# Kernel optimization log

Measured on AMD Instinct MI355X. Metric: run time of the kernel, lower is better.

The kernel has to match this reference:

```python
import jax, jax.numpy as jnp
import numpy as np

B, C, H, W, HID = 4, 32, 256, 256, 64
EPS = 1e-5


def setup_inputs() -> dict:
    key = jax.random.key(0)
    ks = jax.random.split(key, 8)
    s = 0.05
    return {
        "x": jax.random.normal(ks[0], (B, C, H, W), jnp.float32),
        "Wqkv": jax.random.normal(ks[1], (3 * C, C), jnp.float32) * s,   # Conv2d 1x1, no bias
        "W1": jax.random.normal(ks[2], (HID, C), jnp.float32) * s,       # Linear(C -> HID)
        "b1": jnp.zeros((HID,), jnp.float32),
        "ln_w": jnp.ones((HID,), jnp.float32),
        "ln_b": jnp.zeros((HID,), jnp.float32),
        "W2": jax.random.normal(ks[3], (C, HID), jnp.float32) * s,       # Linear(HID -> C)
        "b2": jnp.zeros((C,), jnp.float32),
        "Wg": jax.random.normal(ks[4], (C, C), jnp.float32) * s,         # gate Conv2d 1x1
        "bg": jnp.zeros((C,), jnp.float32),
    }


def _unfold3x3(t):
    # t: (b, c, h, w) -> (b, c, 9, h, w), zero-padded 3x3 neighbors,
    # neighbor order matches F.unfold row-major kernel order.
    b, c, h, w = t.shape
    tp = jnp.pad(t, ((0, 0), (0, 0), (1, 1), (1, 1)))
    return jnp.stack(
        [tp[:, :, dy:dy + h, dx:dx + w] for dy in range(3) for dx in range(3)],
        axis=2,
    )


def reference(x, Wqkv, W1, b1, ln_w, ln_b, W2, b2, Wg, bg):
    b, c, h, w = x.shape
    qkv = jnp.einsum('oc,bchw->bohw', Wqkv, x)
    q, k, v = jnp.split(qkv, 3, axis=1)

    k_un = _unfold3x3(k)  # (b, c, 9, h, w)
    v_un = _unfold3x3(v)

    # (b, h, w, 9, c)
    q_minus_k = jnp.transpose(q[:, :, None] - k_un, (0, 3, 4, 2, 1))

    hid = jnp.einsum('bhwnc,dc->bhwnd', q_minus_k, W1) + b1
    mean = hid.mean(-1, keepdims=True)
    std = jnp.sqrt(((hid - mean) ** 2).mean(-1, keepdims=True))  # unbiased=False
    hid = ln_w * ((hid - mean) / (std + EPS)) + ln_b
    hid = jax.nn.relu(hid)
    scores = jnp.einsum('bhwnd,cd->bhwnc', hid, W2) + b2

    attn = jax.nn.softmax(scores, axis=-2)  # over neighbor dim (9)
    neighbors_v = jnp.transpose(v_un, (0, 3, 4, 2, 1))  # (b, h, w, 9, c)
    weighted_v = jnp.sum(neighbors_v * attn, axis=3)     # (b, h, w, c)
    weighted_v = jnp.transpose(weighted_v, (0, 3, 1, 2)) # (b, c, h, w)

    base = jnp.einsum('oc,bchw->bohw', Wg, x) + bg[None, :, None, None]
    return weighted_v + base + x
```

## Files before the change

kernel.cpp:

```cpp
#include <hip/hip_runtime.h>


#define HWm 65536
#define NPIX 262144
#define PW 258
#define PHW 66564
#define LOG2E 1.44269504088896340736f

typedef __attribute__((ext_vector_type(8))) _Float16 half8;
typedef __attribute__((ext_vector_type(2))) _Float16 half2v;
typedef __attribute__((ext_vector_type(4))) float f32x4;

__device__ __forceinline__ unsigned pkh(float a, float b) {
    auto h = __builtin_amdgcn_cvt_pkrtz(a, b);
    return __builtin_bit_cast(unsigned, h);
}
__device__ __forceinline__ half2v h2(unsigned u) { return __builtin_bit_cast(half2v, u); }

__global__ __launch_bounds__(256) void prep_kernel(
    const float* __restrict__ Wqkv, const float* __restrict__ W1,
    const float* __restrict__ W2, const float* __restrict__ b1v,
    const float* __restrict__ Wg, const float* __restrict__ bgv,
    const float* __restrict__ lnw, const float* __restrict__ lnb,
    const float* __restrict__ b2, float* __restrict__ Wk1,
    float* __restrict__ Wq1, unsigned* __restrict__ W2A,
    unsigned* __restrict__ waA, float* __restrict__ biasF,
    unsigned* __restrict__ beta2G, float* __restrict__ b2adj)
{
    const int tid = threadIdx.x;
    for (int i = tid; i < 2048; i += 256) {
        const int d = i >> 5, c = i & 31;
        float aq = 0.f, ak = 0.f;
#pragma unroll
        for (int k = 0; k < 32; ++k) {
            const float w1 = W1[d * 32 + k];
            aq = fmaf(w1, Wqkv[k * 32 + c], aq);
            ak = fmaf(w1, Wqkv[(32 + k) * 32 + c], ak);
        }
        Wq1[i] = aq;
        Wk1[i] = ak;
    }
    for (int i = tid; i < 1024; i += 256) {
        const int w = i & 3;
        const int lane = (i >> 2) & 63;
        const int kb = (i >> 8) & 1;
        const int ct = (i >> 9) & 1;
        const int row = (lane & 15) + 16 * ct;
        const int k0 = kb * 32 + ((lane >> 4) & 3) * 8 + 2 * w;
        const float s0 = (fabsf(lnw[k0]) < 1e-8f) ? 0.f : lnw[k0] * LOG2E;
        const float s1 = (fabsf(lnw[k0 + 1]) < 1e-8f) ? 0.f : lnw[k0 + 1] * LOG2E;
        W2A[i] = pkh(W2[row * 64 + k0] * s0, W2[row * 64 + k0 + 1] * s1);
    }
    for (int i = tid; i < 32; i += 256) {
        const float w0 = lnw[2 * i], w1 = lnw[2 * i + 1];
        const float be0 = (fabsf(w0) < 1e-8f) ? 0.f : lnb[2 * i] / w0;
        const float be1 = (fabsf(w1) < 1e-8f) ? 0.f : lnb[2 * i + 1] / w1;
        beta2G[i] = pkh(be0, be1);
    }
    for (int i = tid; i < 32; i += 256) {
        float acc = b2[i] * LOG2E;
        for (int d = 0; d < 64; ++d)
            if (fabsf(lnw[d]) < 1e-8f)
                acc += W2[i * 64 + d] * fmaxf(lnb[d], 0.f) * LOG2E;
        b2adj[i] = acc;
    }
    __syncthreads();
    for (int i = tid; i < 3072; i += 256) {
        const int t = i >> 8;
        const int l = (i >> 2) & 63;
        const int w2 = i & 3;
        const int row = 16 * t + (l & 15);
        const int k0 = ((l >> 4) & 3) * 8 + 2 * w2;
        float a0, a1;
        if (row < 64)        { a0 = Wk1[row * 32 + k0];            a1 = Wk1[row * 32 + k0 + 1]; }
        else if (row < 128)  { a0 = Wq1[(row - 64) * 32 + k0];     a1 = Wq1[(row - 64) * 32 + k0 + 1]; }
        else if (row < 160)  { a0 = Wqkv[(row - 64) * 32 + k0];    a1 = Wqkv[(row - 64) * 32 + k0 + 1]; }
        else {
            const int gr = row - 160;
            a0 = Wg[gr * 32 + k0]     + ((gr == k0)     ? 1.f : 0.f);
            a1 = Wg[gr * 32 + k0 + 1] + ((gr == k0 + 1) ? 1.f : 0.f);
        }
        waA[i] = pkh(a0, a1);
    }
    for (int i = tid; i < 3072; i += 256) {
        const int t = i >> 8;
        const int l = (i >> 2) & 63;
        const int r = i & 3;
        const int row = 16 * t + ((l >> 4) & 3) * 4 + r;
        float bv = 0.f;
        if (row >= 64 && row < 128) bv = b1v[row - 64];
        else if (row >= 160)        bv = bgv[row - 160];
        biasF[i] = bv;
    }
}

__global__ __launch_bounds__(256) void kv_kernel(
    const float* __restrict__ x, const half8* __restrict__ waA,
    const float4* __restrict__ biasF, unsigned* __restrict__ khP,
    unsigned* __restrict__ qhg, unsigned* __restrict__ vP,
    float* __restrict__ SkP, float* __restrict__ SqG,
    float* __restrict__ out)
{
    const int bid = blockIdx.x;
    const int tid = threadIdx.x;

    if (bid >= 1024) {
        const int t = (bid - 1024) * 256 + tid;
        if (t < 4112) {
            const int bb = t / 1028;
            const int rr = t - bb * 1028;
            int hh, ww;
            if (rr < 258)      { hh = 0;             ww = rr; }
            else if (rr < 516) { hh = 257;           ww = rr - 258; }
            else if (rr < 772) { hh = rr - 516 + 1;  ww = 0; }
            else               { hh = rr - 772 + 1;  ww = 257; }
            const size_t pixP = (size_t)bb * PHW + hh * PW + ww;
            uint4* kp = (uint4*)khP + pixP * 8;
            uint4* vp = (uint4*)vP + pixP * 4;
            const uint4 z = { 0u, 0u, 0u, 0u };
#pragma unroll
            for (int i = 0; i < 8; ++i) kp[i] = z;
#pragma unroll
            for (int i = 0; i < 4; ++i) vp[i] = z;
            SkP[pixP] = 0.f;
        }
        return;
    }

    __shared__ __align__(16) unsigned xT[256 * 16];

    const int b = bid >> 8;
    const int h = bid & 255;
    const int pix0 = bid * 256;
    const int rowP0 = b * PHW + (h + 1) * PW + 1;

    {
        const float* xp = x + (size_t)b * (32 * HWm) + h * 256 + tid;
        float xv[32];
#pragma unroll
        for (int c = 0; c < 32; ++c) xv[c] = xp[c * HWm];
        unsigned* myx = &xT[tid * 16];
#pragma unroll
        for (int cc = 0; cc < 4; ++cc) {
            uint4 u;
            u.x = pkh(xv[cc * 8 + 0], xv[cc * 8 + 1]);
            u.y = pkh(xv[cc * 8 + 2], xv[cc * 8 + 3]);
            u.z = pkh(xv[cc * 8 + 4], xv[cc * 8 + 5]);
            u.w = pkh(xv[cc * 8 + 6], xv[cc * 8 + 7]);
            *(uint4*)(myx + (((cc + tid) & 3) * 4)) = u;
        }
    }

    const int l = tid & 63;
    const int wid = tid >> 6;
    const int g = l >> 4;
    const int c15 = l & 15;

    half8 A[12];
    f32x4 bF[12];
#pragma unroll
    for (int t = 0; t < 12; ++t) {
        A[t] = waA[t * 64 + l];
        const float4 bv = biasF[t * 64 + l];
        bF[t][0] = bv.x; bF[t][1] = bv.y; bF[t][2] = bv.z; bF[t][3] = bv.w;
    }

#pragma unroll
    for (int pp = 0; pp < 4; ++pp) {
        const int pg = wid * 4 + pp;
        const int px = pg * 16 + c15;
        const half8 bfrag = *(const half8*)&xT[px * 16 + (((g + px) & 3) * 4)];

        f32x4 Ct[12];
#pragma unroll
        for (int t = 0; t < 12; ++t)
            Ct[t] = __builtin_amdgcn_mfma_f32_16x16x32_f16(A[t], bfrag, bF[t], 0, 0, 0);

        const size_t pixP = (size_t)(rowP0 + px);
        const int pixg = pix0 + px;

        float sk = 0.f;
        {
            char* krec = (char*)khP + pixP * 128 + g * 8;
#pragma unroll
            for (int t = 0; t < 4; ++t) {
                uint2 uu;
                uu.x = pkh(Ct[t][0], Ct[t][1]);
                uu.y = pkh(Ct[t][2], Ct[t][3]);
                *(uint2*)(krec + t * 32) = uu;
                sk += (Ct[t][0] + Ct[t][1]) + (Ct[t][2] + Ct[t][3]);
            }
        }
        float sq = 0.f;
        {
            char* qrec = (char*)qhg + (size_t)pixg * 128 + g * 8;
#pragma unroll
            for (int t = 4; t < 8; ++t) {
                uint2 uu;
                uu.x = pkh(Ct[t][0], Ct[t][1]);
                uu.y = pkh(Ct[t][2], Ct[t][3]);
                *(uint2*)(qrec + (t - 4) * 32) = uu;
                sq += (Ct[t][0] + Ct[t][1]) + (Ct[t][2] + Ct[t][3]);
            }
        }
        {
            char* vrec = (char*)vP + pixP * 64 + g * 8;
#pragma unroll
            for (int t = 8; t < 10; ++t) {
                uint2 uu;
                uu.x = pkh(Ct[t][0], Ct[t][1]);
                uu.y = pkh(Ct[t][2], Ct[t][3]);
                *(uint2*)(vrec + (t - 8) * 32) = uu;
            }
        }
        {
            float* op = out + (size_t)b * (32 * HWm) + h * 256 + px;
#pragma unroll
            for (int t = 10; t < 12; ++t) {
#pragma unroll
                for (int r = 0; r < 4; ++r)
                    op[(16 * (t - 10) + g * 4 + r) * HWm] = Ct[t][r];
            }
        }
        sk += __shfl_xor(sk, 16);
        sk += __shfl_xor(sk, 32);
        sq += __shfl_xor(sq, 16);
        sq += __shfl_xor(sq, 32);
        if (g == 0) {
            SkP[pixP] = sk;
            SqG[pixg] = sq;
        }
    }
}

__global__ __launch_bounds__(512) void attn_kernel(
    const unsigned* __restrict__ qhg, const unsigned* __restrict__ khP,
    const unsigned* __restrict__ vP, const half8* __restrict__ w2a,
    const float* __restrict__ SkP, const float* __restrict__ SqG,
    const unsigned* __restrict__ beta2G, const float* __restrict__ b2adj,
    float* __restrict__ out)
{
    __shared__ __align__(16) char hidL[65536];

    const int tid = threadIdx.x;
    const int grp = tid >> 8;
    const int p = tid & 255;

    const int bid = blockIdx.x;
    const int swz = (bid & 7) * 128 + (bid >> 3);
    const int b = swz >> 8;
    const int trem = swz & 255;
    const int h0 = (trem >> 4) << 4;
    const int w0 = (trem & 15) << 4;

    const int l = tid & 63;
    const int lane15 = p & 15;
    const int q = (p >> 4) & 3;
    const int wrow = (p >> 6) & 3;

    const int row = p >> 4;
    const int h = h0 + row, w = w0 + lane15;
    const int pix = (b << 16) + (h << 8) + w;
    const int pixP = b * PHW + (h + 1) * PW + (w + 1);
    const int tileP = b * PHW + (h0 + 1) * PW + (w0 + 1);

    unsigned qw[32];
    {
        const uint4* qp = (const uint4*)qhg + (size_t)pix * 8;
#pragma unroll
        for (int i = 0; i < 8; ++i) {
            const uint4 u = qp[i];
            qw[4 * i] = u.x; qw[4 * i + 1] = u.y; qw[4 * i + 2] = u.z; qw[4 * i + 3] = u.w;
        }
    }
    const float Sq = SqG[pix];

    const half8 a00 = w2a[0 * 64 + l];
    const half8 a01 = w2a[1 * 64 + l];
    const half8 a10 = w2a[2 * 64 + l];
    const half8 a11 = w2a[3 * 64 + l];

    float b2v[8];
    {
        const float4 t0 = *(const float4*)(b2adj + q * 4);
        const float4 t1 = *(const float4*)(b2adj + 16 + q * 4);
        b2v[0] = t0.x; b2v[1] = t0.y; b2v[2] = t0.z; b2v[3] = t0.w;
        b2v[4] = t1.x; b2v[5] = t1.y; b2v[6] = t1.z; b2v[7] = t1.w;
    }

    float ssum[32], wv[32];
#pragma unroll
    for (int i = 0; i < 32; ++i) { ssum[i] = 0.f; wv[i] = 0.f; }

    const uint4* khP4 = (const uint4*)khP;
    char* const grpbase = hidL + (grp << 15);
    char* const myhid = grpbase + p * 128;
    const int myswz = (p & 7) << 4;
    const half2v zero2 = { (_Float16)0.f, (_Float16)0.f };

    const int n_start = grp ? 4 : 0;
    const int n_end = grp ? 9 : 4;

    for (int n = n_start; n < n_end; ++n) {
        const int dy = n / 3 - 1, dx = n % 3 - 1;

        const int nofs = pixP + dy * PW + dx;
        const uint4* kp = khP4 + (size_t)nofs * 8;
        const float Sk = SkP[nofs];
        float ss0 = 0.f, ss1 = 0.f;
        half2v hd2[32];
#pragma unroll
        for (int cj = 0; cj < 8; ++cj) {
            const uint4 kc = kp[cj];
            hd2[cj * 4 + 0] = h2(qw[cj * 4 + 0]) - h2(kc.x);
            hd2[cj * 4 + 1] = h2(qw[cj * 4 + 1]) - h2(kc.y);
            hd2[cj * 4 + 2] = h2(qw[cj * 4 + 2]) - h2(kc.z);
            hd2[cj * 4 + 3] = h2(qw[cj * 4 + 3]) - h2(kc.w);
            ss0 = __builtin_amdgcn_fdot2(hd2[cj * 4 + 0], hd2[cj * 4 + 0], ss0, false);
            ss1 = __builtin_amdgcn_fdot2(hd2[cj * 4 + 1], hd2[cj * 4 + 1], ss1, false);
            ss0 = __builtin_amdgcn_fdot2(hd2[cj * 4 + 2], hd2[cj * 4 + 2], ss0, false);
            ss1 = __builtin_amdgcn_fdot2(hd2[cj * 4 + 3], hd2[cj * 4 + 3], ss1, false);
        }
        const float sum = Sq - Sk;
        const float sumsq = ss0 + ss1;
        const float mean = sum * 0.015625f;
        float var = fmaf(-mean, mean, sumsq * 0.015625f);
        var = fmaxf(var, 0.f);
        const float inv = __builtin_amdgcn_rcpf(sqrtf(var) + 1e-5f);
        const float nmi = -mean * inv;
        const half2v inv2 = { (_Float16)inv, (_Float16)inv };
        const half2v nmi2 = { (_Float16)nmi, (_Float16)nmi };

#pragma unroll
        for (int cj = 0; cj < 8; ++cj) {
            unsigned ou[4];
#pragma unroll
            for (int j = 0; j < 4; ++j) {
                half2v nb = h2(beta2G[cj * 4 + j]) + nmi2;
                half2v u = __builtin_elementwise_fma(hd2[cj * 4 + j], inv2, nb);
                u = __builtin_elementwise_max(u, zero2);
                ou[j] = __builtin_bit_cast(unsigned, u);
            }
            uint4 o;
            o.x = ou[0]; o.y = ou[1]; o.z = ou[2]; o.w = ou[3];
            *(uint4*)(myhid + ((cj * 16) ^ myswz)) = o;
        }

#pragma unroll
        for (int gg = 0; gg < 4; ++gg) {
            const int g = wrow * 4 + gg;
            const int px = g * 16 + lane15;
            const char* bp = grpbase + px * 128;
            const int sw = (lane15 & 7) << 4;
            const half8 b0 = *(const half8*)(bp + ((q * 16) ^ sw));
            const half8 b1 = *(const half8*)(bp + (((4 + q) * 16) ^ sw));
            f32x4 acc0 = { b2v[0], b2v[1], b2v[2], b2v[3] };
            f32x4 acc1 = { b2v[4], b2v[5], b2v[6], b2v[7] };
            acc0 = __builtin_amdgcn_mfma_f32_16x16x32_f16(a00, b0, acc0, 0, 0, 0);
            acc0 = __builtin_amdgcn_mfma_f32_16x16x32_f16(a01, b1, acc0, 0, 0, 0);
            acc1 = __builtin_amdgcn_mfma_f32_16x16x32_f16(a10, b0, acc1, 0, 0, 0);
            acc1 = __builtin_amdgcn_mfma_f32_16x16x32_f16(a11, b1, acc1, 0, 0, 0);

            const int npP = tileP + (g + dy) * PW + (lane15 + dx);
            const unsigned* vp = vP + (size_t)npP * 16;
            const uint2 vA = *(const uint2*)(vp + q * 2);
            const uint2 vB = *(const uint2*)(vp + 8 + q * 2);
            const half2v va0 = h2(vA.x), va1 = h2(vA.y);
            const half2v vb0 = h2(vB.x), vb1 = h2(vB.y);
            const float va[4] = { (float)va0[0], (float)va0[1], (float)va1[0], (float)va1[1] };
            const float vb[4] = { (float)vb0[0], (float)vb0[1], (float)vb1[0], (float)vb1[1] };
#pragma unroll
            for (int r = 0; r < 4; ++r) {
                const float e0 = __builtin_amdgcn_exp2f(acc0[r]);
                ssum[gg * 8 + r] += e0;
                wv[gg * 8 + r] = fmaf(e0, va[r], wv[gg * 8 + r]);
                const float e1 = __builtin_amdgcn_exp2f(acc1[r]);
                ssum[gg * 8 + 4 + r] += e1;
                wv[gg * 8 + 4 + r] = fmaf(e1, vb[r], wv[gg * 8 + 4 + r]);
            }
        }
    }

    __syncthreads();
    if (grp == 1) {
#pragma unroll
        for (int j = 0; j < 8; ++j) {
            *(float4*)(hidL + j * 4096 + p * 16) =
                make_float4(wv[j * 4], wv[j * 4 + 1], wv[j * 4 + 2], wv[j * 4 + 3]);
        }
#pragma unroll
        for (int j = 0; j < 8; ++j) {
            *(float4*)(hidL + (8 + j) * 4096 + p * 16) =
                make_float4(ssum[j * 4], ssum[j * 4 + 1], ssum[j * 4 + 2], ssum[j * 4 + 3]);
        }
    }
    __syncthreads();
    if (grp == 0) {
#pragma unroll
        for (int j = 0; j < 8; ++j) {
            const float4 t = *(const float4*)(hidL + j * 4096 + p * 16);
            wv[j * 4] += t.x; wv[j * 4 + 1] += t.y; wv[j * 4 + 2] += t.z; wv[j * 4 + 3] += t.w;
        }
#pragma unroll
        for (int j = 0; j < 8; ++j) {
            const float4 t = *(const float4*)(hidL + (8 + j) * 4096 + p * 16);
            ssum[j * 4] += t.x; ssum[j * 4 + 1] += t.y; ssum[j * 4 + 2] += t.z; ssum[j * 4 + 3] += t.w;
        }
#pragma unroll
        for (int gg = 0; gg < 4; ++gg) {
            const int g = wrow * 4 + gg;
            float* op = out + (size_t)b * (32 * HWm) + ((h0 + g) << 8) + (w0 + lane15);
#pragma unroll
            for (int r = 0; r < 4; ++r) {
                const int ch0 = q * 4 + r;
                const int ch1 = 16 + q * 4 + r;
                op[ch0 * HWm] += wv[gg * 8 + r] * __builtin_amdgcn_rcpf(ssum[gg * 8 + r]);
                op[ch1 * HWm] += wv[gg * 8 + 4 + r] * __builtin_amdgcn_rcpf(ssum[gg * 8 + 4 + r]);
            }
        }
    }
}

extern "C" void kernel_launch(void* const* d_in, const int* in_sizes, int n_in,
                              void* d_out, int out_size, void* d_ws, size_t ws_size,
                              hipStream_t stream) {
    const float* x    = (const float*)d_in[0];
    const float* Wqkv = (const float*)d_in[1];
    const float* W1   = (const float*)d_in[2];
    const float* b1   = (const float*)d_in[3];
    const float* lnw  = (const float*)d_in[4];
    const float* lnb  = (const float*)d_in[5];
    const float* W2   = (const float*)d_in[6];
    const float* b2   = (const float*)d_in[7];
    const float* Wg   = (const float*)d_in[8];
    const float* bg   = (const float*)d_in[9];
    float* out = (float*)d_out;

    float* ws  = (float*)d_ws;
    float* Wk1 = ws;
    float* Wq1 = ws + 2048;
    unsigned* W2A  = (unsigned*)(ws + 4096);
    unsigned* waA  = (unsigned*)(ws + 5120);
    float*    biasF = ws + 8192;
    unsigned* beta2G = (unsigned*)(ws + 11264);
    float*    b2adj  = ws + 11296;
    unsigned* khP = (unsigned*)(ws + 11328);
    unsigned* qhg = khP + (size_t)4 * PHW * 32;
    unsigned* vP  = qhg + (size_t)NPIX * 32;
    float* SkP = (float*)(vP + (size_t)4 * PHW * 16);
    float* SqG = SkP + (size_t)4 * PHW;

    prep_kernel<<<1, 256, 0, stream>>>(Wqkv, W1, W2, b1, Wg, bg, lnw, lnb, b2,
                                       Wk1, Wq1, W2A, waA, biasF, beta2G, b2adj);
    kv_kernel<<<1024 + 17, 256, 0, stream>>>(x, (const half8*)waA,
                                             (const float4*)biasF,
                                             khP, qhg, vP, SkP, SqG, out);
    attn_kernel<<<1024, 512, 0, stream>>>(qhg, khP, vP, (const half8*)W2A,
                                          SkP, SqG, beta2G, b2adj, out);
}
```

Before: 129.2 us.

## Accumulate softmax in packed fp16, prefetch next neighbor keys, stage diffs in LDS

Measured after the change: 172.2 us. 1.33x slower.

```diff
diff --git a/kernel.cpp b/kernel.cpp
--- a/kernel.cpp
+++ b/kernel.cpp
@@ -16,6 +16,7 @@
     return __builtin_bit_cast(unsigned, h);
 }
 __device__ __forceinline__ half2v h2(unsigned u) { return __builtin_bit_cast(half2v, u); }
+__device__ __forceinline__ unsigned u2(half2v h) { return __builtin_bit_cast(unsigned, h); }
 
 __global__ __launch_bounds__(256) void prep_kernel(
     const float* __restrict__ Wqkv, const float* __restrict__ W1,
@@ -263,6 +264,7 @@
     const int pix = (b << 16) + (h << 8) + w;
     const int pixP = b * PHW + (h + 1) * PW + (w + 1);
     const int tileP = b * PHW + (h0 + 1) * PW + (w0 + 1);
+    const int vbase0 = tileP + lane15;
 
     unsigned qw[32];
     {
@@ -288,38 +290,59 @@
         b2v[4] = t1.x; b2v[5] = t1.y; b2v[6] = t1.z; b2v[7] = t1.w;
     }
 
-    float ssum[32], wv[32];
-#pragma unroll
-    for (int i = 0; i < 32; ++i) { ssum[i] = 0.f; wv[i] = 0.f; }
+    half2v wv2[16], ssum2[16];
+    const half2v zero2 = { (_Float16)0.f, (_Float16)0.f };
+#pragma unroll
+    for (int i = 0; i < 16; ++i) { wv2[i] = zero2; ssum2[i] = zero2; }
 
     const uint4* khP4 = (const uint4*)khP;
     char* const grpbase = hidL + (grp << 15);
     char* const myhid = grpbase + p * 128;
     const int myswz = (p & 7) << 4;
-    const half2v zero2 = { (_Float16)0.f, (_Float16)0.f };
-
-    const int n_start = grp ? 4 : 0;
-    const int n_end = grp ? 9 : 4;
-
-    for (int n = n_start; n < n_end; ++n) {
-        const int dy = n / 3 - 1, dx = n % 3 - 1;
-
-        const int nofs = pixP + dy * PW + dx;
-        const uint4* kp = khP4 + (size_t)nofs * 8;
-        const float Sk = SkP[nofs];
+
+    const int cnt = grp ? 5 : 4;
+    int relOff = grp ? 0 : (-PW - 1);
+    int m3 = grp ? 1 : 0;
+    int nofs = pixP + relOff;
+
+    uint4 kc[8];
+    {
+        const uint4* kp0 = khP4 + (size_t)nofs * 8;
+#pragma unroll
+        for (int j = 0; j < 8; ++j) kc[j] = kp0[j];
+    }
+    float Sk = SkP[nofs];
+
+#pragma unroll
+    for (int nn = 0; nn < 5; ++nn) {
+        if (nn >= cnt) break;
+
+        const int step = (m3 == 2) ? (PW - 2) : 1;
+        const int nofsN = nofs + step;
+        uint4 kn[8];
+        float SkN = 0.f;
+        if (nn + 1 < cnt) {
+            const uint4* kp = khP4 + (size_t)nofsN * 8;
+#pragma unroll
+            for (int j = 0; j < 8; ++j) kn[j] = kp[j];
+            SkN = SkP[nofsN];
+        }
+
         float ss0 = 0.f, ss1 = 0.f;
-        half2v hd2[32];
 #pragma unroll
         for (int cj = 0; cj < 8; ++cj) {
-            const uint4 kc = kp[cj];
-            hd2[cj * 4 + 0] = h2(qw[cj * 4 + 0]) - h2(kc.x);
-            hd2[cj * 4 + 1] = h2(qw[cj * 4 + 1]) - h2(kc.y);
-            hd2[cj * 4 + 2] = h2(qw[cj * 4 + 2]) - h2(kc.z);
-            hd2[cj * 4 + 3] = h2(qw[cj * 4 + 3]) - h2(kc.w);
-            ss0 = __builtin_amdgcn_fdot2(hd2[cj * 4 + 0], hd2[cj * 4 + 0], ss0, false);
-            ss1 = __builtin_amdgcn_fdot2(hd2[cj * 4 + 1], hd2[cj * 4 + 1], ss1, false);
-            ss0 = __builtin_amdgcn_fdot2(hd2[cj * 4 + 2], hd2[cj * 4 + 2], ss0, false);
-            ss1 = __builtin_amdgcn_fdot2(hd2[cj * 4 + 3], hd2[cj * 4 + 3], ss1, false);
+            const uint4 kcv = kc[cj];
+            const half2v d0 = h2(qw[cj * 4 + 0]) - h2(kcv.x);
+            const half2v d1 = h2(qw[cj * 4 + 1]) - h2(kcv.y);
+            const half2v d2 = h2(qw[cj * 4 + 2]) - h2(kcv.z);
+            const half2v d3 = h2(qw[cj * 4 + 3]) - h2(kcv.w);
+            ss0 = __builtin_amdgcn_fdot2(d0, d0, ss0, false);
+            ss1 = __builtin_amdgcn_fdot2(d1, d1, ss1, false);
+            ss0 = __builtin_amdgcn_fdot2(d2, d2, ss0, false);
+            ss1 = __builtin_amdgcn_fdot2(d3, d3, ss1, false);
+            uint4 o;
+            o.x = u2(d0); o.y = u2(d1); o.z = u2(d2); o.w = u2(d3);
+            *(uint4*)(myhid + ((cj * 16) ^ myswz)) = o;
         }
         const float sum = Sq - Sk;
         const float sumsq = ss0 + ss1;
@@ -333,17 +356,19 @@
 
 #pragma unroll
         for (int cj = 0; cj < 8; ++cj) {
-            unsigned ou[4];
+            char* pp = myhid + ((cj * 16) ^ myswz);
+            const uint4 t = *(const uint4*)pp;
+            uint4 o;
 #pragma unroll
             for (int j = 0; j < 4; ++j) {
+                const unsigned tw = (j == 0) ? t.x : (j == 1) ? t.y : (j == 2) ? t.z : t.w;
                 half2v nb = h2(beta2G[cj * 4 + j]) + nmi2;
-                half2v u = __builtin_elementwise_fma(hd2[cj * 4 + j], inv2, nb);
+                half2v u = __builtin_elementwise_fma(h2(tw), inv2, nb);
                 u = __builtin_elementwise_max(u, zero2);
-                ou[j] = __builtin_bit_cast(unsigned, u);
+                const unsigned uo = u2(u);
+                if (j == 0) o.x = uo; else if (j == 1) o.y = uo; else if (j == 2) o.z = uo; else o.w = uo;
             }
-            uint4 o;
-            o.x = ou[0]; o.y = ou[1]; o.z = ou[2]; o.w = ou[3];
-            *(uint4*)(myhid + ((cj * 16) ^ myswz)) = o;
+            *(uint4*)pp = o;
         }
 
 #pragma unroll
@@ -361,50 +386,63 @@
             acc1 = __builtin_amdgcn_mfma_f32_16x16x32_f16(a10, b0, acc1, 0, 0, 0);
             acc1 = __builtin_amdgcn_mfma_f32_16x16x32_f16(a11, b1, acc1, 0, 0, 0);
 
-            const int npP = tileP + (g + dy) * PW + (lane15 + dx);
+            const int npP = vbase0 + g * PW + relOff;
             const unsigned* vp = vP + (size_t)npP * 16;
             const uint2 vA = *(const uint2*)(vp + q * 2);
             const uint2 vB = *(const uint2*)(vp + 8 + q * 2);
-            const half2v va0 = h2(vA.x), va1 = h2(vA.y);
-            const half2v vb0 = h2(vB.x), vb1 = h2(vB.y);
-            const float va[4] = { (float)va0[0], (float)va0[1], (float)va1[0], (float)va1[1] };
-            const float vb[4] = { (float)vb0[0], (float)vb0[1], (float)vb1[0], (float)vb1[1] };
-#pragma unroll
-            for (int r = 0; r < 4; ++r) {
-                const float e0 = __builtin_amdgcn_exp2f(acc0[r]);
-                ssum[gg * 8 + r] += e0;
-                wv[gg * 8 + r] = fmaf(e0, va[r], wv[gg * 8 + r]);
-                const float e1 = __builtin_amdgcn_exp2f(acc1[r]);
-                ssum[gg * 8 + 4 + r] += e1;
-                wv[gg * 8 + 4 + r] = fmaf(e1, vb[r], wv[gg * 8 + 4 + r]);
-            }
-        }
+
+            const half2v e01 = h2(pkh(__builtin_amdgcn_exp2f(acc0[0]), __builtin_amdgcn_exp2f(acc0[1])));
+            const half2v e23 = h2(pkh(__builtin_amdgcn_exp2f(acc0[2]), __builtin_amdgcn_exp2f(acc0[3])));
+            const half2v f01 = h2(pkh(__builtin_amdgcn_exp2f(acc1[0]), __builtin_amdgcn_exp2f(acc1[1])));
+            const half2v f23 = h2(pkh(__builtin_amdgcn_exp2f(acc1[2]), __builtin_amdgcn_exp2f(acc1[3])));
+            ssum2[gg * 4 + 0] += e01;
+            ssum2[gg * 4 + 1] += e23;
+            ssum2[gg * 4 + 2] += f01;
+            ssum2[gg * 4 + 3] += f23;
+            wv2[gg * 4 + 0] = __builtin_elementwise_fma(e01, h2(vA.x), wv2[gg * 4 + 0]);
+            wv2[gg * 4 + 1] = __builtin_elementwise_fma(e23, h2(vA.y), wv2[gg * 4 + 1]);
+            wv2[gg * 4 + 2] = __builtin_elementwise_fma(f01, h2(vB.x), wv2[gg * 4 + 2]);
+            wv2[gg * 4 + 3] = __builtin_elementwise_fma(f23, h2(vB.y), wv2[gg * 4 + 3]);
+        }
+
+#pragma unroll
+        for (int j = 0; j < 8; ++j) kc[j] = kn[j];
+        Sk = SkN;
+        nofs = nofsN;
+        relOff += step;
+        m3 = (m3 == 2) ? 0 : m3 + 1;
     }
 
     __syncthreads();
     if (grp == 1) {
 #pragma unroll
-        for (int j = 0; j < 8; ++j) {
-            *(float4*)(hidL + j * 4096 + p * 16) =
-                make_float4(wv[j * 4], wv[j * 4 + 1], wv[j * 4 + 2], wv[j * 4 + 3]);
-        }
-#pragma unroll
-        for (int j = 0; j < 8; ++j) {
-            *(float4*)(hidL + (8 + j) * 4096 + p * 16) =
-                make_float4(ssum[j * 4], ssum[j * 4 + 1], ssum[j * 4 + 2], ssum[j * 4 + 3]);
+        for (int j4 = 0; j4 < 4; ++j4) {
+            uint4 o;
+            o.x = u2(wv2[j4 * 4 + 0]); o.y = u2(wv2[j4 * 4 + 1]);
+            o.z = u2(wv2[j4 * 4 + 2]); o.w = u2(wv2[j4 * 4 + 3]);
+            *(uint4*)(hidL + j4 * 4096 + p * 16) = o;
+        }
+#pragma unroll
+        for (int j4 = 0; j4 < 4; ++j4) {
+            uint4 o;
+            o.x = u2(ssum2[j4 * 4 + 0]); o.y = u2(ssum2[j4 * 4 + 1]);
+            o.z = u2(ssum2[j4 * 4 + 2]); o.w = u2(ssum2[j4 * 4 + 3]);
+            *(uint4*)(hidL + (4 + j4) * 4096 + p * 16) = o;
         }
     }
     __syncthreads();
     if (grp == 0) {
 #pragma unroll
-        for (int j = 0; j < 8; ++j) {
-            const float4 t = *(const float4*)(hidL + j * 4096 + p * 16);
-            wv[j * 4] += t.x; wv[j * 4 + 1] += t.y; wv[j * 4 + 2] += t.z; wv[j * 4 + 3] += t.w;
-        }
-#pragma unroll
-        for (int j = 0; j < 8; ++j) {
-            const float4 t = *(const float4*)(hidL + (8 + j) * 4096 + p * 16);
-            ssum[j * 4] += t.x; ssum[j * 4 + 1] += t.y; ssum[j * 4 + 2] += t.z; ssum[j * 4 + 3] += t.w;
+        for (int j4 = 0; j4 < 4; ++j4) {
+            const uint4 t = *(const uint4*)(hidL + j4 * 4096 + p * 16);
+            wv2[j4 * 4 + 0] += h2(t.x); wv2[j4 * 4 + 1] += h2(t.y);
+            wv2[j4 * 4 + 2] += h2(t.z); wv2[j4 * 4 + 3] += h2(t.w);
+        }
+#pragma unroll
+        for (int j4 = 0; j4 < 4; ++j4) {
+            const uint4 t = *(const uint4*)(hidL + (4 + j4) * 4096 + p * 16);
+            ssum2[j4 * 4 + 0] += h2(t.x); ssum2[j4 * 4 + 1] += h2(t.y);
+            ssum2[j4 * 4 + 2] += h2(t.z); ssum2[j4 * 4 + 3] += h2(t.w);
         }
 #pragma unroll
         for (int gg = 0; gg < 4; ++gg) {
@@ -414,8 +452,12 @@
             for (int r = 0; r < 4; ++r) {
                 const int ch0 = q * 4 + r;
                 const int ch1 = 16 + q * 4 + r;
-                op[ch0 * HWm] += wv[gg * 8 + r] * __builtin_amdgcn_rcpf(ssum[gg * 8 + r]);
-                op[ch1 * HWm] += wv[gg * 8 + 4 + r] * __builtin_amdgcn_rcpf(ssum[gg * 8 + 4 + r]);
+                const float w0v = (float)((r < 2) ? wv2[gg * 4 + 0][r] : wv2[gg * 4 + 1][r - 2]);
+                const float s0v = (float)((r < 2) ? ssum2[gg * 4 + 0][r] : ssum2[gg * 4 + 1][r - 2]);
+                const float w1v = (float)((r < 2) ? wv2[gg * 4 + 2][r] : wv2[gg * 4 + 3][r - 2]);
+                const float s1v = (float)((r < 2) ? ssum2[gg * 4 + 2][r] : ssum2[gg * 4 + 3][r - 2]);
+                op[ch0 * HWm] += w0v * __builtin_amdgcn_rcpf(s0v);
+                op[ch1 * HWm] += w1v * __builtin_amdgcn_rcpf(s1v);
             }
         }
     }
```
